# Kernel tuning notes

Measured on AMD Instinct MI355X. Metric: run time of the kernel, lower is better.

Reference implementation:

```python
import jax, jax.numpy as jnp
import numpy as np

NUM_HEADS = 16

def setup_inputs() -> dict:
    key = jax.random.key(0)
    ks = jax.random.split(key, 8)
    L, S, N, E = 2048, 2048, 2, 1024
    return {
        "query": jax.random.normal(ks[0], (L, N, E), jnp.float32),
        "key": jax.random.normal(ks[1], (S, N, E), jnp.float32),
        "value": jax.random.normal(ks[2], (S, N, E), jnp.float32),
        "in_proj_weight": jax.random.normal(ks[3], (3 * E, E), jnp.float32) * (E ** -0.5),
        "in_proj_bias": jax.random.normal(ks[4], (3 * E,), jnp.float32) * 0.01,
        "out_proj_weight": jax.random.normal(ks[5], (E, E), jnp.float32) * (E ** -0.5),
        "out_proj_bias": jax.random.normal(ks[6], (E,), jnp.float32) * 0.01,
        "rel_bias": jax.random.normal(ks[7], (NUM_HEADS, 2 * S - 1), jnp.float32) * 0.02,
    }


def reference(query, key, value, in_proj_weight, in_proj_bias,
              out_proj_weight, out_proj_bias, rel_bias):
    L, N, E = query.shape
    S = key.shape[0]
    H = NUM_HEADS
    D = E // H
    scaling = D ** -0.5

    # in-projection: F.linear(x, W, b) = x @ W.T + b, with W split into q/k/v rows
    wq, wk, wv = jnp.split(in_proj_weight, 3, axis=0)
    bq, bk, bv = jnp.split(in_proj_bias, 3, axis=0)
    q = (query @ wq.T + bq) * scaling          # [L,N,E]
    k = key @ wk.T + bk                        # [S,N,E]
    v = value @ wv.T + bv                      # [S,N,E]

    q = q.reshape(L, N, H, D)
    k = k.reshape(S, N, H, D)
    v = v.reshape(S, N, H, D)

    # attention scores [N,H,L,S]
    scores = jnp.einsum("lnhd,snhd->nhls", q, k)

    # relative-position bias: bias[h,i,j] = rel_bias[h, (i - j) + S - 1]
    rel_idx = jnp.arange(L)[:, None] - jnp.arange(S)[None, :] + (S - 1)  # [L,S]
    bias = rel_bias[:, rel_idx]                # [H,L,S]
    scores = scores + bias[None, :, :, :]

    attn = jax.nn.softmax(scores, axis=-1)     # [N,H,L,S]

    out = jnp.einsum("nhls,snhd->lnhd", attn, v).reshape(L, N, E)
    out = out @ out_proj_weight.T + out_proj_bias  # [L,N,E]
    return out
```

## Files before the change

### kernel.cpp

```cpp
#include <hip/hip_runtime.h>
#include <hip/hip_bf16.h>


typedef __attribute__((ext_vector_type(8))) short bf16x8;
typedef __attribute__((ext_vector_type(4))) float f32x4;
typedef __attribute__((ext_vector_type(16))) float f32x16;
typedef __attribute__((ext_vector_type(4))) unsigned int u32x4;

#define LOG2E 1.4426950408889634f

__device__ __forceinline__ unsigned short f2bf(float x) {
  unsigned u = __float_as_uint(x);
  u += 0x7fffu + ((u >> 16) & 1u);
  return (unsigned short)(u >> 16);
}

__device__ __forceinline__ void gld_lds16(const void* g, void* l) {
  __builtin_amdgcn_global_load_lds(
      (const __attribute__((address_space(1))) unsigned int*)g,
      (__attribute__((address_space(3))) unsigned int*)l,
      16, 0, 0);
}

__global__ __launch_bounds__(256) void cvt_qkv(const float* __restrict__ q,
                                               const float* __restrict__ k,
                                               const float* __restrict__ v,
                                               unsigned short* __restrict__ dst) {
  const int z = blockIdx.y;
  const float* src = (z == 0) ? q : (z == 1) ? k : v;
  int i = blockIdx.x * 256 + threadIdx.x;
  float4 vv = reinterpret_cast<const float4*>(src)[i];
  ushort4 o;
  o.x = f2bf(vv.x); o.y = f2bf(vv.y); o.z = f2bf(vv.z); o.w = f2bf(vv.w);
  reinterpret_cast<ushort4*>(dst + (size_t)z * 4194304)[i] = o;
}

__global__ __launch_bounds__(256) void cvt_w(const float* __restrict__ w_in,
                                             const float* __restrict__ w_out,
                                             unsigned short* __restrict__ wIn,
                                             unsigned short* __restrict__ wOut) {
  int i = blockIdx.x * 256 + threadIdx.x;
  if (i < 786432) {
    float scale = (i < 262144) ? 0.125f * LOG2E : 1.0f;
    float4 vv = reinterpret_cast<const float4*>(w_in)[i];
    ushort4 o;
    o.x = f2bf(vv.x * scale); o.y = f2bf(vv.y * scale);
    o.z = f2bf(vv.z * scale); o.w = f2bf(vv.w * scale);
    reinterpret_cast<ushort4*>(wIn)[i] = o;
  } else {
    int j = i - 786432;
    float4 vv = reinterpret_cast<const float4*>(w_out)[j];
    ushort4 o;
    o.x = f2bf(vv.x); o.y = f2bf(vv.y); o.z = f2bf(vv.z); o.w = f2bf(vv.w);
    reinterpret_cast<ushort4*>(wOut)[j] = o;
  }
}

template<int OUT_F32, int QKV>
__global__ __launch_bounds__(256) void gemm_nt(const unsigned short* __restrict__ Abase,
                                               const unsigned short* __restrict__ Wbase,
                                               const float* __restrict__ biasBase,
                                               void* __restrict__ outBase) {
  const int K = 1024, Nout = 1024;
  __shared__ __attribute__((aligned(16))) unsigned short As[2][128 * 32];
  __shared__ __attribute__((aligned(16))) unsigned short Bs[2][128 * 32];

  const int tid = threadIdx.x;
  const int l = tid & 63, w = tid >> 6;
  const int lane15 = tid & 15, lhi = (tid >> 4) & 3;
  const int Mbase = blockIdx.y * 128, Nbase = blockIdx.x * 128;
  const int rb = (w >> 1) * 64, cb = (w & 1) * 64;

  const unsigned short* A = Abase;
  const unsigned short* W = Wbase;
  const float* bias = biasBase;
  float biasScale = 1.0f;
  unsigned short* outU = (unsigned short*)outBase;
  float* outF = (float*)outBase;
  if (QKV) {
    const int z = blockIdx.z;
    A    += (size_t)z * 4194304;
    W    += (size_t)z * 1048576;
    bias += z * 1024;
    outU += (size_t)z * 4194304;
    if (z == 0) biasScale = 0.125f * LOG2E;
  }

  auto stage = [&](int kt, int buf) {
#pragma unroll
    for (int i = 0; i < 2; ++i) {
      int u = (i * 4 + w) * 64 + l;
      int row = u >> 2, slot = u & 3;
      int ks = slot ^ ((row >> 1) & 3);
      gld_lds16(A + (size_t)(Mbase + row) * K + kt * 32 + ks * 8,
                &As[buf][(i * 4 + w) * 512]);
      gld_lds16(W + (size_t)(Nbase + row) * K + kt * 32 + ks * 8,
                &Bs[buf][(i * 4 + w) * 512]);
    }
  };

  f32x4 acc[4][4] = {};
  stage(0, 0);
  const int NK = 32;
  for (int kt = 0; kt < NK; ++kt) {
    __syncthreads();
    if (kt + 1 < NK) stage(kt + 1, (kt + 1) & 1);
    const int buf = kt & 1;
    bf16x8 a[4], b[4];
#pragma unroll
    for (int m = 0; m < 4; ++m) {
      int row = rb + m * 16 + lane15;
      a[m] = *(const bf16x8*)&As[buf][row * 32 + (lhi ^ ((row >> 1) & 3)) * 8];
      int col = cb + m * 16 + lane15;
      b[m] = *(const bf16x8*)&Bs[buf][col * 32 + (lhi ^ ((col >> 1) & 3)) * 8];
    }
#pragma unroll
    for (int m = 0; m < 4; ++m)
#pragma unroll
      for (int nt = 0; nt < 4; ++nt)
        acc[m][nt] = __builtin_amdgcn_mfma_f32_16x16x32_bf16(a[m], b[nt], acc[m][nt], 0, 0, 0);
  }

  float bv[4];
#pragma unroll
  for (int nt = 0; nt < 4; ++nt)
    bv[nt] = bias[Nbase + cb + nt * 16 + lane15] * biasScale;
#pragma unroll
  for (int m = 0; m < 4; ++m)
#pragma unroll
    for (int nt = 0; nt < 4; ++nt)
#pragma unroll
      for (int r = 0; r < 4; ++r) {
        float v = acc[m][nt][r] + bv[nt];
        size_t idx = (size_t)(Mbase + rb + m * 16 + lhi * 4 + r) * Nout +
                     (Nbase + cb + nt * 16 + lane15);
        if (OUT_F32) outF[idx] = v;
        else         outU[idx] = f2bf(v);
      }
}

__global__ __launch_bounds__(256) void vtrans(const unsigned short* __restrict__ vP,
                                              unsigned short* __restrict__ vT) {
  __shared__ unsigned short t_lds[64][66];
  const int tid = threadIdx.x;
  const int st = blockIdx.x, nh = blockIdx.y;
  const int n = nh >> 4, h = nh & 15;
  const int sb = st * 64;
#pragma unroll
  for (int r = 0; r < 2; ++r) {
    int idx = tid + r * 256;
    int row = idx >> 3, ch = idx & 7;
    bf16x8 v = *(const bf16x8*)(vP + (size_t)((sb + row) * 2 + n) * 1024 + h * 64 + ch * 8);
#pragma unroll
    for (int j = 0; j < 8; ++j) t_lds[row][ch * 8 + j] = (unsigned short)v[j];
  }
  __syncthreads();
#pragma unroll
  for (int r = 0; r < 2; ++r) {
    int idx = tid + r * 256;
    int d = idx >> 3, sc = idx & 7;
    bf16x8 o;
#pragma unroll
    for (int j = 0; j < 8; ++j) o[j] = (short)t_lds[sc * 8 + j][d];
    *(bf16x8*)(vT + (size_t)(nh * 64 + d) * 2048 + sb + sc * 8) = o;
  }
}

__global__ __launch_bounds__(256) void attn(const unsigned short* __restrict__ qP,
                                            const unsigned short* __restrict__ kP,
                                            const unsigned short* __restrict__ vT,
                                            const float* __restrict__ rel_bias,
                                            unsigned short* __restrict__ attnout) {
  __shared__ __attribute__((aligned(16))) unsigned short bias4[4 * 2208];
  __shared__ __attribute__((aligned(16))) unsigned short Ks[2][4096];
  __shared__ __attribute__((aligned(16))) unsigned short Vs[2][4096];

  const int tid = threadIdx.x;
  const int l = tid & 63, w = tid >> 6;
  const int l31 = tid & 31, lh5 = (tid >> 5) & 1;
  const int bid = blockIdx.y * 16 + blockIdx.x;
  const int qt = bid >> 5;
  const int nh = (bid & 7) * 4 + ((bid >> 3) & 3);
  const int n = nh >> 4, h = nh & 15;
  const int qb = qt * 128;
  const int wq = w * 32;
  const int lloc = wq + l31;

  for (int i2 = tid; i2 < 1104; i2 += 256) {
#pragma unroll
    for (int m = 0; m < 4; ++m) {
      int s0 = qb + 2 * i2 + m;
      float f0 = (s0 <= 4094) ? rel_bias[h * 4095 + s0] * LOG2E : 0.f;
      float f1 = (s0 + 1 <= 4094) ? rel_bias[h * 4095 + s0 + 1] * LOG2E : 0.f;
      unsigned pk;
      asm("v_cvt_pk_bf16_f32 %0, %1, %2" : "=v"(pk) : "v"(f0), "v"(f1));
      *(unsigned*)&bias4[m * 2208 + 2 * i2] = pk;
    }
  }

  bf16x8 qf[4];
  {
    const unsigned short* qrow = qP + (size_t)((qb + lloc) * 2 + n) * 1024 + h * 64;
#pragma unroll
    for (int m16 = 0; m16 < 4; ++m16)
      qf[m16] = *(const bf16x8*)(qrow + m16 * 16 + lh5 * 8);
  }

  const short one_bf = (short)0x3F80;
  bf16x8 ones = {one_bf, one_bf, one_bf, one_bf, one_bf, one_bf, one_bf, one_bf};

  f32x16 o0 = {}, o1 = {}, osum = {};

  auto stage = [&](int kt, int buf) {
#pragma unroll
    for (int i = 0; i < 2; ++i) {
      int u = (i * 4 + w) * 64 + l;
      int row = u >> 3, slot = u & 7;
      int ks = slot ^ (row & 7);
      gld_lds16(kP + (size_t)((kt * 64 + row) * 2 + n) * 1024 + h * 64 + ks * 8,
                &Ks[buf][(i * 4 + w) * 512]);
      gld_lds16(vT + (size_t)(nh * 64 + row) * 2048 + kt * 64 + ks * 8,
                &Vs[buf][(i * 4 + w) * 512]);
    }
  };

  stage(0, 0);
  for (int kt = 0; kt < 32; ++kt) {
    __syncthreads();
    if (kt + 1 < 32) stage(kt + 1, (kt + 1) & 1);
    const int buf = kt & 1;

#pragma unroll
    for (int sb = 0; sb < 2; ++sb) {
      const int srow = sb * 32 + l31;
      bf16x8 kf[4];
#pragma unroll
      for (int m16 = 0; m16 < 4; ++m16)
        kf[m16] = *(const bf16x8*)&Ks[buf][srow * 64 + (((m16 * 2 + lh5) ^ (srow & 7)) * 8)];

      f32x16 c;
#pragma unroll
      for (int rg = 0; rg < 4; ++rg) {
        int a = lloc + 2047 - (kt * 64 + sb * 32 + rg * 8 + lh5 * 4) - 3;
        const uint2 dd = *(const uint2*)&bias4[(a & 3) * 2208 + (a & ~3)];
        c[rg * 4 + 0] = __uint_as_float(dd.y & 0xFFFF0000u);
        c[rg * 4 + 1] = __uint_as_float(dd.y << 16);
        c[rg * 4 + 2] = __uint_as_float(dd.x & 0xFFFF0000u);
        c[rg * 4 + 3] = __uint_as_float(dd.x << 16);
      }

#pragma unroll
      for (int m16 = 0; m16 < 4; ++m16)
        c = __builtin_amdgcn_mfma_f32_32x32x16_bf16(kf[m16], qf[m16], c, 0, 0, 0);

      float p[16];
#pragma unroll
      for (int i = 0; i < 16; ++i)
        asm("v_exp_f32 %0, %1" : "=v"(p[i]) : "v"(c[i]));

      unsigned pk0[4], pk1[4];
#pragma unroll
      for (int rg = 0; rg < 4; ++rg) {
        asm("v_cvt_pk_bf16_f32 %0, %1, %2" : "=v"(pk0[rg]) : "v"(p[rg * 4 + 0]), "v"(p[rg * 4 + 1]));
        asm("v_cvt_pk_bf16_f32 %0, %1, %2" : "=v"(pk1[rg]) : "v"(p[rg * 4 + 2]), "v"(p[rg * 4 + 3]));
      }

#pragma unroll
      for (int t = 0; t < 2; ++t) {
        unsigned x0 = pk0[t * 2 + 0], y0 = pk0[t * 2 + 1];
        unsigned x1 = pk1[t * 2 + 0], y1 = pk1[t * 2 + 1];
        asm("v_permlane32_swap_b32 %0, %1" : "+v"(x0), "+v"(y0));
        asm("v_permlane32_swap_b32 %0, %1" : "+v"(x1), "+v"(y1));
        u32x4 pu; pu[0] = x0; pu[1] = x1; pu[2] = y0; pu[3] = y1;
        bf16x8 pa = __builtin_bit_cast(bf16x8, pu);
        const int tb = sb * 2 + t;
#pragma unroll
        for (int dn = 0; dn < 2; ++dn) {
          int drow = dn * 32 + l31;
          bf16x8 vf = *(const bf16x8*)&Vs[buf][drow * 64 + (((tb * 2 + lh5) ^ (drow & 7)) * 8)];
          if (dn == 0) o0 = __builtin_amdgcn_mfma_f32_32x32x16_bf16(pa, vf, o0, 0, 0, 0);
          else         o1 = __builtin_amdgcn_mfma_f32_32x32x16_bf16(pa, vf, o1, 0, 0, 0);
        }
        osum = __builtin_amdgcn_mfma_f32_32x32x16_bf16(pa, ones, osum, 0, 0, 0);
      }
    }
  }

#pragma unroll
  for (int reg = 0; reg < 16; ++reg) {
    float inv = 1.0f / osum[reg];
    int lrow = qb + wq + (reg & 3) + 8 * (reg >> 2) + 4 * lh5;
    size_t base = (size_t)(lrow * 2 + n) * 1024 + h * 64 + l31;
    attnout[base]      = f2bf(o0[reg] * inv);
    attnout[base + 32] = f2bf(o1[reg] * inv);
  }
}

extern "C" void kernel_launch(void* const* d_in, const int* in_sizes, int n_in,
                              void* d_out, int out_size, void* d_ws, size_t ws_size,
                              hipStream_t stream) {
  (void)in_sizes; (void)n_in; (void)out_size; (void)ws_size;
  const float* query = (const float*)d_in[0];
  const float* key   = (const float*)d_in[1];
  const float* value = (const float*)d_in[2];
  const float* w_in  = (const float*)d_in[3];
  const float* b_in  = (const float*)d_in[4];
  const float* w_out = (const float*)d_in[5];
  const float* b_out = (const float*)d_in[6];
  const float* rel_b = (const float*)d_in[7];

  unsigned short* ws   = (unsigned short*)d_ws;
  unsigned short* qkvA = ws;
  unsigned short* wIn  = ws + 12582912;
  unsigned short* wOut = ws + 15728640;
  unsigned short* qP   = ws + 16777216;
  unsigned short* vT   = ws + 29360128;
  unsigned short* attnout = qkvA;

  dim3 gC(4096, 3);
  cvt_qkv<<<gC, 256, 0, stream>>>(query, key, value, qkvA);
  cvt_w<<<4096, 256, 0, stream>>>(w_in, w_out, wIn, wOut);

  dim3 gQKV(8, 32, 3);
  gemm_nt<0, 1><<<gQKV, 256, 0, stream>>>(qkvA, wIn, b_in, qP);

  dim3 g32(32, 32);
  vtrans<<<g32, 256, 0, stream>>>(qP + 2 * 4194304, vT);
  dim3 gA(16, 32);
  attn<<<gA, 256, 0, stream>>>(qP, qP + 4194304, vT, rel_b, attnout);

  dim3 gOUT(8, 32, 1);
  gemm_nt<1, 0><<<gOUT, 256, 0, stream>>>(attnout, wOut, b_out, d_out);
}
```

Before: 243.5 us.

## Split attention over key halves with a combine kernel to double block count

The attention kernel now splits the key sequence into two halves via a third grid dimension. Each half writes unnormalized partial outputs and row sums, and a new combine kernel adds them and normalizes. The aim is to double the block count from 512 to 1024 so the GPU's compute units are better occupied, and to shrink the bias LDS buffer. The LDS swizzle also gains an extra XOR term, likely to reduce bank conflicts. The cost is an extra kernel launch plus a round trip through memory for the bf16 partials, which adds rounding error since the partials are unnormalized. The sums buffer reuses the wIn workspace, which is safe only because the in-projection GEMM has already consumed it.

```diff
diff --git a/kernel.cpp b/kernel.cpp
--- a/kernel.cpp
+++ b/kernel.cpp
@@ -8,6 +8,7 @@
 typedef __attribute__((ext_vector_type(4))) unsigned int u32x4;
 
 #define LOG2E 1.4426950408889634f
+#define BSTR 1184
 
 __device__ __forceinline__ unsigned short f2bf(float x) {
   unsigned u = __float_as_uint(x);
@@ -170,8 +171,9 @@
                                             const unsigned short* __restrict__ kP,
                                             const unsigned short* __restrict__ vT,
                                             const float* __restrict__ rel_bias,
-                                            unsigned short* __restrict__ attnout) {
-  __shared__ __attribute__((aligned(16))) unsigned short bias4[4 * 2208];
+                                            unsigned short* __restrict__ opart,
+                                            float* __restrict__ sums) {
+  __shared__ __attribute__((aligned(16))) unsigned short bias4[4 * BSTR];
   __shared__ __attribute__((aligned(16))) unsigned short Ks[2][4096];
   __shared__ __attribute__((aligned(16))) unsigned short Vs[2][4096];
 
@@ -181,20 +183,23 @@
   const int bid = blockIdx.y * 16 + blockIdx.x;
   const int qt = bid >> 5;
   const int nh = (bid & 7) * 4 + ((bid >> 3) & 3);
+  const int shalf = blockIdx.z;
   const int n = nh >> 4, h = nh & 15;
   const int qb = qt * 128;
   const int wq = w * 32;
   const int lloc = wq + l31;
-
-  for (int i2 = tid; i2 < 1104; i2 += 256) {
+  const int kt0 = shalf * 16;
+  const int woff = (1 - shalf) * 1024;
+
+  for (int i2 = tid; i2 < 592; i2 += 256) {
 #pragma unroll
     for (int m = 0; m < 4; ++m) {
-      int s0 = qb + 2 * i2 + m;
+      int s0 = qb + woff + 2 * i2 + m;
       float f0 = (s0 <= 4094) ? rel_bias[h * 4095 + s0] * LOG2E : 0.f;
       float f1 = (s0 + 1 <= 4094) ? rel_bias[h * 4095 + s0 + 1] * LOG2E : 0.f;
       unsigned pk;
       asm("v_cvt_pk_bf16_f32 %0, %1, %2" : "=v"(pk) : "v"(f0), "v"(f1));
-      *(unsigned*)&bias4[m * 2208 + 2 * i2] = pk;
+      *(unsigned*)&bias4[m * BSTR + 2 * i2] = pk;
     }
   }
 
@@ -216,7 +221,7 @@
     for (int i = 0; i < 2; ++i) {
       int u = (i * 4 + w) * 64 + l;
       int row = u >> 3, slot = u & 7;
-      int ks = slot ^ (row & 7);
+      int ks = slot ^ (row & 7) ^ ((row >> 1) & 4);
       gld_lds16(kP + (size_t)((kt * 64 + row) * 2 + n) * 1024 + h * 64 + ks * 8,
                 &Ks[buf][(i * 4 + w) * 512]);
       gld_lds16(vT + (size_t)(nh * 64 + row) * 2048 + kt * 64 + ks * 8,
@@ -224,11 +229,12 @@
     }
   };
 
-  stage(0, 0);
-  for (int kt = 0; kt < 32; ++kt) {
+  stage(kt0, 0);
+  for (int ktl = 0; ktl < 16; ++ktl) {
+    const int kt = kt0 + ktl;
     __syncthreads();
-    if (kt + 1 < 32) stage(kt + 1, (kt + 1) & 1);
-    const int buf = kt & 1;
+    if (ktl + 1 < 16) stage(kt + 1, (ktl + 1) & 1);
+    const int buf = ktl & 1;
 
 #pragma unroll
     for (int sb = 0; sb < 2; ++sb) {
@@ -236,13 +242,14 @@
       bf16x8 kf[4];
 #pragma unroll
       for (int m16 = 0; m16 < 4; ++m16)
-        kf[m16] = *(const bf16x8*)&Ks[buf][srow * 64 + (((m16 * 2 + lh5) ^ (srow & 7)) * 8)];
+        kf[m16] = *(const bf16x8*)&Ks[buf][srow * 64 +
+                   (((m16 * 2 + lh5) ^ (srow & 7) ^ ((srow >> 1) & 4)) * 8)];
 
       f32x16 c;
 #pragma unroll
       for (int rg = 0; rg < 4; ++rg) {
-        int a = lloc + 2047 - (kt * 64 + sb * 32 + rg * 8 + lh5 * 4) - 3;
-        const uint2 dd = *(const uint2*)&bias4[(a & 3) * 2208 + (a & ~3)];
+        int a = lloc + 2044 - (kt * 64 + sb * 32 + rg * 8 + lh5 * 4) - woff;
+        const uint2 dd = *(const uint2*)&bias4[(a & 3) * BSTR + (a & ~3)];
         c[rg * 4 + 0] = __uint_as_float(dd.y & 0xFFFF0000u);
         c[rg * 4 + 1] = __uint_as_float(dd.y << 16);
         c[rg * 4 + 2] = __uint_as_float(dd.x & 0xFFFF0000u);
@@ -277,7 +284,8 @@
 #pragma unroll
         for (int dn = 0; dn < 2; ++dn) {
           int drow = dn * 32 + l31;
-          bf16x8 vf = *(const bf16x8*)&Vs[buf][drow * 64 + (((tb * 2 + lh5) ^ (drow & 7)) * 8)];
+          bf16x8 vf = *(const bf16x8*)&Vs[buf][drow * 64 +
+                       (((tb * 2 + lh5) ^ (drow & 7) ^ ((drow >> 1) & 4)) * 8)];
           if (dn == 0) o0 = __builtin_amdgcn_mfma_f32_32x32x16_bf16(pa, vf, o0, 0, 0, 0);
           else         o1 = __builtin_amdgcn_mfma_f32_32x32x16_bf16(pa, vf, o1, 0, 0, 0);
         }
@@ -288,12 +296,38 @@
 
 #pragma unroll
   for (int reg = 0; reg < 16; ++reg) {
-    float inv = 1.0f / osum[reg];
     int lrow = qb + wq + (reg & 3) + 8 * (reg >> 2) + 4 * lh5;
-    size_t base = (size_t)(lrow * 2 + n) * 1024 + h * 64 + l31;
-    attnout[base]      = f2bf(o0[reg] * inv);
-    attnout[base + 32] = f2bf(o1[reg] * inv);
-  }
+    size_t base = (size_t)shalf * 4194304 + (size_t)(lrow * 2 + n) * 1024 + h * 64 + l31;
+    opart[base]      = f2bf(o0[reg]);
+    opart[base + 32] = f2bf(o1[reg]);
+  }
+  if (l31 == 0) {
+#pragma unroll
+    for (int reg = 0; reg < 16; ++reg) {
+      int lrow = qb + wq + (reg & 3) + 8 * (reg >> 2) + 4 * lh5;
+      sums[shalf * 65536 + (lrow * 2 + n) * 16 + h] = osum[reg];
+    }
+  }
+}
+
+__global__ __launch_bounds__(256) void combine(const unsigned short* __restrict__ opart,
+                                               const float* __restrict__ sums,
+                                               unsigned short* __restrict__ attnout) {
+  int idx = blockIdx.x * 256 + threadIdx.x;
+  int t = idx >> 7;
+  int e = (idx & 127) * 8;
+  int h = e >> 6;
+  float inv = 1.0f / (sums[t * 16 + h] + sums[65536 + t * 16 + h]);
+  const bf16x8 a = *(const bf16x8*)&opart[(size_t)t * 1024 + e];
+  const bf16x8 b = *(const bf16x8*)&opart[4194304 + (size_t)t * 1024 + e];
+  bf16x8 r;
+#pragma unroll
+  for (int j = 0; j < 8; ++j) {
+    float fa = __uint_as_float((unsigned)(unsigned short)a[j] << 16);
+    float fb = __uint_as_float((unsigned)(unsigned short)b[j] << 16);
+    r[j] = (short)f2bf((fa + fb) * inv);
+  }
+  *(bf16x8*)&attnout[(size_t)t * 1024 + e] = r;
 }
 
 extern "C" void kernel_launch(void* const* d_in, const int* in_sizes, int n_in,
@@ -316,6 +350,8 @@
   unsigned short* qP   = ws + 16777216;
   unsigned short* vT   = ws + 29360128;
   unsigned short* attnout = qkvA;
+  unsigned short* opart   = qkvA + 4194304;
+  float*          sums    = (float*)wIn;
 
   dim3 gC(4096, 3);
   cvt_qkv<<<gC, 256, 0, stream>>>(query, key, value, qkvA);
@@ -326,8 +362,9 @@
 
   dim3 g32(32, 32);
   vtrans<<<g32, 256, 0, stream>>>(qP + 2 * 4194304, vT);
-  dim3 gA(16, 32);
-  attn<<<gA, 256, 0, stream>>>(qP, qP + 4194304, vT, rel_b, attnout);
+  dim3 gA(16, 32, 2);
+  attn<<<gA, 256, 0, stream>>>(qP, qP + 4194304, vT, rel_b, opart, sums);
+  combine<<<2048, 256, 0, stream>>>(opart, sums, attnout);
 
   dim3 gOUT(8, 32, 1);
   gemm_nt<1, 0><<<gOUT, 256, 0, stream>>>(attnout, wOut, b_out, d_out);
```

Result: slower. 253.6 us (+4.1%).
